# Kernel tuning notes

Hardware: AMD Instinct MI355X
Metric: run time of the kernel (lower is better)

The kernel has to match this reference:

```python
import jax, jax.numpy as jnp
import numpy as np

D_MODEL = 256
LAMBDA_DECAY = 0.5
NEG_INF = -1e9


def setup_inputs() -> dict:
    key = jax.random.key(0)
    k0, k1, k2, k3 = jax.random.split(key, 4)
    B, S = 8, 2048
    inputs = jax.random.normal(k0, (B, S, 2), dtype=jnp.float32)
    # Dense(d_model, use_bias=False) on a scalar feature -> weight [1, d_model]
    Wq = jax.random.normal(k1, (1, D_MODEL), dtype=jnp.float32) * 0.05
    Wk = jax.random.normal(k2, (1, D_MODEL), dtype=jnp.float32) * 0.05
    Wv = jax.random.normal(k3, (1, D_MODEL), dtype=jnp.float32) * 0.05
    return {"inputs": inputs, "Wq": Wq, "Wk": Wk, "Wv": Wv}


def reference(inputs, Wq, Wk, Wv):
    sizes = inputs[:, :, 0]    # [B, S]
    heights = inputs[:, :, 1]  # [B, S]
    h = heights[:, :, None]    # [B, S, 1]
    q = h * Wq[0]              # [B, S, d] (scalar-feature dense)
    k = h * Wk[0]
    v = h * Wv[0]
    dk = jnp.asarray(q.shape[-1], dtype=q.dtype)
    logits = jnp.einsum('bsd,btd->bst', q, k) / jnp.sqrt(dk)  # [B, S, S]
    # additive distance penalty from pairwise |size_i - size_j|
    penalty = -LAMBDA_DECAY * jnp.abs(sizes[:, :, None] - sizes[:, None, :])
    logits = logits + penalty
    # mask branch: valid where heights != 0
    attn_mask = (heights != 0).astype(logits.dtype)  # [B, S]
    key_mask = attn_mask[:, None, :]                 # [B, 1, S]
    query_mask = attn_mask[:, :, None]               # [B, S, 1]
    logits = logits + (1.0 - key_mask) * NEG_INF
    logits = logits + (1.0 - query_mask) * NEG_INF
    weights = jax.nn.softmax(logits, axis=-1)
    weights = weights * key_mask
    out = jnp.einsum('bst,btd->bsd', weights, v)  # [B, S, d]
    return out
```

## Files before the change

### kernel.cpp

```cpp
#include <hip/hip_runtime.h>

#define SEQ 2048
#define DM  256
#define WAVES_PER_BLOCK 8
#define THREADS (WAVES_PER_BLOCK * 64)

__global__ __launch_bounds__(THREADS) void dwsa_kernel(
    const float* __restrict__ in,
    const float* __restrict__ Wq,
    const float* __restrict__ Wk,
    const float* __restrict__ Wv,
    float* __restrict__ out)
{
    __shared__ float4 sv4[SEQ / 2];

    const int tid  = threadIdx.x;
    const int lane = tid & 63;
    const int wave = tid >> 6;

    const int blocks_per_b = SEQ / WAVES_PER_BLOCK;
    const int b  = blockIdx.x / blocks_per_b;
    const int s0 = (blockIdx.x % blocks_per_b) * WAVES_PER_BLOCK;

    const float4* inb4 = (const float4*)(in + (size_t)b * SEQ * 2);
    #pragma unroll
    for (int t = tid; t < SEQ / 2; t += THREADS) sv4[t] = inb4[t];

    float cpart = 0.0f;
    #pragma unroll
    for (int j = 0; j < 4; ++j) {
        const int i = lane + 64 * j;
        cpart = fmaf(Wq[i], Wk[i], cpart);
    }
    #pragma unroll
    for (int off = 32; off; off >>= 1) cpart += __shfl_xor(cpart, off);
    const float c_l2e = cpart * (1.0f / 16.0f) * 1.44269504f;
    const float half_l2e = 0.72134752f;

    const float4 wv = ((const float4*)Wv)[lane];

    __syncthreads();

    const int s = s0 + wave;
    const float2 me = ((const float2*)sv4)[s];
    const float ss   = me.x;
    const float chs  = c_l2e * me.y;

    float se = 0.0f, seh = 0.0f;
    #pragma unroll
    for (int i = 0; i < SEQ / 128; ++i) {
        const float4 kt = sv4[lane + 64 * i];
        {
            const float d = fabsf(ss - kt.x);
            float e = __builtin_amdgcn_exp2f(fmaf(chs, kt.y, -half_l2e * d));
            e = (kt.y == 0.0f) ? 0.0f : e;
            se += e;
            seh = fmaf(e, kt.y, seh);
        }
        {
            const float d = fabsf(ss - kt.z);
            float e = __builtin_amdgcn_exp2f(fmaf(chs, kt.w, -half_l2e * d));
            e = (kt.w == 0.0f) ? 0.0f : e;
            se += e;
            seh = fmaf(e, kt.w, seh);
        }
    }
    #pragma unroll
    for (int off = 32; off; off >>= 1) {
        se  += __shfl_xor(se, off);
        seh += __shfl_xor(seh, off);
    }
    const float A = seh / se;

    float4 o;
    o.x = A * wv.x; o.y = A * wv.y; o.z = A * wv.z; o.w = A * wv.w;
    ((float4*)(out + ((size_t)b * SEQ + s) * DM))[lane] = o;
}

extern "C" void kernel_launch(void* const* d_in, const int* in_sizes, int n_in,
                              void* d_out, int out_size, void* d_ws, size_t ws_size,
                              hipStream_t stream) {
    const float* in = (const float*)d_in[0];
    const float* Wq = (const float*)d_in[1];
    const float* Wk = (const float*)d_in[2];
    const float* Wv = (const float*)d_in[3];
    float* out = (float*)d_out;

    const int B = in_sizes[0] / (SEQ * 2);
    dim3 grid(B * (SEQ / WAVES_PER_BLOCK));
    dwsa_kernel<<<grid, THREADS, 0, stream>>>(in, Wq, Wk, Wv, out);
}
```

Before: 16.79 us.

## Process four query rows per wave and fold masking into prescaled sizes

Each wave now computes four query rows, so each shared-memory key load is reused across four rows of exp/accumulate work. Key sizes are prescaled by half·log2e when staged into shared memory. Masked keys get a huge sentinel size so their exp2 underflows to zero, which removes the per-element select. The trade-offs are fewer total waves and more registers per thread. The sentinel also changes the result for a zero-height query row (output becomes zero), which the reference does not do, though random inputs never contain exact zeros.

```diff
diff --git a/kernel.cpp b/kernel.cpp
--- a/kernel.cpp
+++ b/kernel.cpp
@@ -2,8 +2,10 @@
 
 #define SEQ 2048
 #define DM  256
-#define WAVES_PER_BLOCK 8
-#define THREADS (WAVES_PER_BLOCK * 64)
+#define WAVES 4
+#define THREADS (WAVES * 64)
+#define RPW 4
+#define ROWS_PER_BLOCK (WAVES * RPW)
 
 __global__ __launch_bounds__(THREADS) void dwsa_kernel(
     const float* __restrict__ in,
@@ -18,13 +20,20 @@
     const int lane = tid & 63;
     const int wave = tid >> 6;
 
-    const int blocks_per_b = SEQ / WAVES_PER_BLOCK;
+    const float HALF_L2E = 0.72134752f;
+
+    const int blocks_per_b = SEQ / ROWS_PER_BLOCK;
     const int b  = blockIdx.x / blocks_per_b;
-    const int s0 = (blockIdx.x % blocks_per_b) * WAVES_PER_BLOCK;
+    const int s0 = (blockIdx.x % blocks_per_b) * ROWS_PER_BLOCK;
 
     const float4* inb4 = (const float4*)(in + (size_t)b * SEQ * 2);
     #pragma unroll
-    for (int t = tid; t < SEQ / 2; t += THREADS) sv4[t] = inb4[t];
+    for (int t = tid; t < SEQ / 2; t += THREADS) {
+        float4 p = inb4[t];
+        p.x = (p.y == 0.0f) ? 7.2e8f : HALF_L2E * p.x;
+        p.z = (p.w == 0.0f) ? 7.2e8f : HALF_L2E * p.z;
+        sv4[t] = p;
+    }
 
     float cpart = 0.0f;
     #pragma unroll
@@ -35,46 +44,55 @@
     #pragma unroll
     for (int off = 32; off; off >>= 1) cpart += __shfl_xor(cpart, off);
     const float c_l2e = cpart * (1.0f / 16.0f) * 1.44269504f;
-    const float half_l2e = 0.72134752f;
 
     const float4 wv = ((const float4*)Wv)[lane];
 
     __syncthreads();
 
-    const int s = s0 + wave;
-    const float2 me = ((const float2*)sv4)[s];
-    const float ss   = me.x;
-    const float chs  = c_l2e * me.y;
+    const int rbase = s0 + wave * RPW;
+    float ssr[RPW], chs[RPW], se[RPW], seh[RPW];
+    #pragma unroll
+    for (int r = 0; r < RPW; ++r) {
+        const float2 me = ((const float2*)sv4)[rbase + r];
+        ssr[r] = me.x;
+        chs[r] = c_l2e * me.y;
+        se[r] = 0.0f; seh[r] = 0.0f;
+    }
 
-    float se = 0.0f, seh = 0.0f;
     #pragma unroll
     for (int i = 0; i < SEQ / 128; ++i) {
         const float4 kt = sv4[lane + 64 * i];
-        {
-            const float d = fabsf(ss - kt.x);
-            float e = __builtin_amdgcn_exp2f(fmaf(chs, kt.y, -half_l2e * d));
-            e = (kt.y == 0.0f) ? 0.0f : e;
-            se += e;
-            seh = fmaf(e, kt.y, seh);
-        }
-        {
-            const float d = fabsf(ss - kt.z);
-            float e = __builtin_amdgcn_exp2f(fmaf(chs, kt.w, -half_l2e * d));
-            e = (kt.w == 0.0f) ? 0.0f : e;
-            se += e;
-            seh = fmaf(e, kt.w, seh);
+        #pragma unroll
+        for (int r = 0; r < RPW; ++r) {
+            {
+                const float dl = ssr[r] - kt.x;
+                const float e  = __builtin_amdgcn_exp2f(fmaf(chs[r], kt.y, -fabsf(dl)));
+                se[r] += e;
+                seh[r] = fmaf(e, kt.y, seh[r]);
+            }
+            {
+                const float dl = ssr[r] - kt.z;
+                const float e  = __builtin_amdgcn_exp2f(fmaf(chs[r], kt.w, -fabsf(dl)));
+                se[r] += e;
+                seh[r] = fmaf(e, kt.w, seh[r]);
+            }
         }
     }
+
     #pragma unroll
-    for (int off = 32; off; off >>= 1) {
-        se  += __shfl_xor(se, off);
-        seh += __shfl_xor(seh, off);
+    for (int r = 0; r < RPW; ++r) {
+        float a = se[r], h = seh[r];
+        #pragma unroll
+        for (int off = 32; off; off >>= 1) {
+            a += __shfl_xor(a, off);
+            h += __shfl_xor(h, off);
+        }
+        a = (a == 0.0f) ? 1.0f : a;
+        const float A = h / a;
+        float4 o;
+        o.x = A * wv.x; o.y = A * wv.y; o.z = A * wv.z; o.w = A * wv.w;
+        ((float4*)(out + ((size_t)b * SEQ + rbase + r) * DM))[lane] = o;
     }
-    const float A = seh / se;
-
-    float4 o;
-    o.x = A * wv.x; o.y = A * wv.y; o.z = A * wv.z; o.w = A * wv.w;
-    ((float4*)(out + ((size_t)b * SEQ + s) * DM))[lane] = o;
 }
 
 extern "C" void kernel_launch(void* const* d_in, const int* in_sizes, int n_in,
@@ -87,6 +105,6 @@
     float* out = (float*)d_out;
 
     const int B = in_sizes[0] / (SEQ * 2);
-    dim3 grid(B * (SEQ / WAVES_PER_BLOCK));
+    dim3 grid(B * (SEQ / ROWS_PER_BLOCK));
     dwsa_kernel<<<grid, THREADS, 0, stream>>>(in, Wq, Wk, Wv, out);
 }
```

Result: faster. 15.69 us (-6.6%).
